# Performance work log

Measured on AMD Instinct MI355X. Metric: run time of the kernel, lower is better.

The kernel has to match this reference:

```python
import jax, jax.numpy as jnp
import numpy as np

L, B, D = 4096, 4, 1024

def setup_inputs() -> dict:
    key = jax.random.key(0)
    k1, k2, k3, k4 = jax.random.split(key, 4)
    return {
        "x": jax.random.normal(k1, (L, B, D), dtype=jnp.float32),
        "lmlg": jax.random.normal(k2, (D,), dtype=jnp.float32),
        "theta": jax.random.normal(k3, (D,), dtype=jnp.float32),
        "last_conv_init": jax.random.normal(k4, (D,), dtype=jnp.float32),
    }

def reference(x, lmlg, theta, last_conv_init):
    seq_len, batch, dim = x.shape
    # per-channel decay*rotation: c = gamma * e^{i*theta}, gamma = exp(-exp(lmlg))
    gamma = jnp.exp(-jnp.exp(lmlg))                       # [D]
    c = gamma * jnp.exp(1j * theta)                       # [D] complex64
    # causal filter c^n for n = 0..L-1
    n = jnp.arange(seq_len)[:, None]                      # [L,1]
    filt = c[None, :] ** n                                # [L,D] complex64
    # linear (causal) convolution via zero-padded FFT of length 2L
    filt_fft = jnp.fft.fft(filt, n=2 * seq_len, axis=0)   # [2L,D]
    x_fft = jnp.fft.fft(x, n=2 * seq_len, axis=0)         # [2L,B,D]
    conv_filter_x = jnp.fft.ifft(filt_fft[:, None, :] * x_fft, axis=0)[:seq_len]  # [L,B,D]
    # carry-in state (fresh state = last_conv_init expanded; detached in torch)
    last_conv = jax.lax.stop_gradient(
        jnp.broadcast_to(last_conv_init.astype(conv_filter_x.dtype), (batch, dim))
    )                                                     # [B,D]
    conv_with_past = conv_filter_x + last_conv[None, :, :] * filt[:, None, :] * c[None, None, :]
    return conv_with_past.real * x
```

## Files before the change

kernel.cpp:

```cpp
#include <hip/hip_runtime.h>


#define L_  4096
#define B_  4
#define D_  1024
#define BD_ (B_ * D_)
#define NC_ 128
#define CH_ (L_ / NC_)

template <int CH>
__global__ __launch_bounds__(256) void sc_sum(
    const float* __restrict__ x,
    const float* __restrict__ lmlg,
    const float* __restrict__ theta,
    float2* __restrict__ ws) {
  const int t   = threadIdx.x;
  const int bid = blockIdx.x;
  const int db  = bid & 3;
  const int b   = (bid >> 2) & (B_ - 1);
  const int k   = bid >> 4;
  const int d   = (db << 8) + t;

  const float lg = lmlg[d], th = theta[d];
  const float g  = expf(-expf(lg));
  const float cr = g * cosf(th), ci = g * sinf(th);

  float sr = 0.f, si = 0.f;
  const float* xp = x + (size_t)k * CH * BD_ + (size_t)b * D_ + d;
#pragma unroll 8
  for (int j = 0; j < CH; ++j) {
    float xv = xp[(size_t)j * BD_];
    float nr = fmaf(cr, sr, fmaf(-ci, si, xv));
    float ni = fmaf(cr, si, ci * sr);
    sr = nr; si = ni;
  }
  ws[(size_t)(k * B_ + b) * D_ + d] = make_float2(sr, si);
}

template <int CH>
__global__ __launch_bounds__(256) void sc_out(
    const float* __restrict__ x,
    const float* __restrict__ lmlg,
    const float* __restrict__ theta,
    const float* __restrict__ init,
    const float2* __restrict__ ws,
    float* __restrict__ out) {
  const int t   = threadIdx.x;
  const int bid = blockIdx.x;
  const int db  = bid & 3;
  const int b   = (bid >> 2) & (B_ - 1);
  const int k   = bid >> 4;
  const int d   = (db << 8) + t;

  const float lg = lmlg[d], th = theta[d];
  const float e  = expf(lg);
  const float g  = expf(-e);
  const float cr = g * cosf(th), ci = g * sinf(th);

  const float chf = (float)CH;
  const float G   = expf(-e * chf);
  const float Cr  = G * cosf(th * chf), Ci = G * sinf(th * chf);

  float hr = init[d], hi = 0.f;
  const float2* sp = ws + (size_t)b * D_ + d;
  {
    const float C2r = fmaf(Cr, Cr, -Ci * Ci);
    const float C2i = 2.f * Cr * Ci;
    int kk = 0;
    for (; kk + 2 <= k; kk += 2) {
      float2 s0 = sp[(size_t)kk * BD_];
      float2 s1 = sp[(size_t)(kk + 1) * BD_];
      float ur = fmaf(Cr, s0.x, fmaf(-Ci, s0.y, s1.x));
      float ui = fmaf(Cr, s0.y, fmaf( Ci, s0.x, s1.y));
      float nr = fmaf(C2r, hr, fmaf(-C2i, hi, ur));
      float ni = fmaf(C2r, hi, fmaf( C2i, hr, ui));
      hr = nr; hi = ni;
    }
    if (kk < k) {
      float2 s = sp[(size_t)kk * BD_];
      float nr = fmaf(Cr, hr, fmaf(-Ci, hi, s.x));
      float ni = fmaf(Cr, hi, fmaf( Ci, hr, s.y));
      hr = nr; hi = ni;
    }
  }

  const size_t off = (size_t)k * CH * BD_ + (size_t)b * D_ + d;
  const float* xp = x + off;
  float*       op = out + off;
#pragma unroll 8
  for (int j = 0; j < CH; ++j) {
    float xv = xp[(size_t)j * BD_];
    float nr = fmaf(cr, hr, fmaf(-ci, hi, xv));
    float ni = fmaf(cr, hi, ci * hr);
    hr = nr; hi = ni;
    __builtin_nontemporal_store(nr * xv, op + (size_t)j * BD_);
  }
}

__global__ __launch_bounds__(256) void sc_full(
    const float* __restrict__ x, const float* __restrict__ lmlg,
    const float* __restrict__ theta, const float* __restrict__ init,
    float* __restrict__ out) {
  const int idx = blockIdx.x * 256 + threadIdx.x;
  const int d   = idx & (D_ - 1);
  float g = expf(-expf(lmlg[d]));
  float cr = g * cosf(theta[d]), ci = g * sinf(theta[d]);
  float hr = init[d], hi = 0.f;
  const float* xp = x + idx;
  float*       op = out + idx;
  for (int n = 0; n < L_; ++n) {
    float xv = xp[(size_t)n * BD_];
    float nr = fmaf(cr, hr, fmaf(-ci, hi, xv));
    float ni = fmaf(cr, hi, ci * hr);
    hr = nr; hi = ni;
    op[(size_t)n * BD_] = nr * xv;
  }
}

extern "C" void kernel_launch(void* const* d_in, const int* in_sizes, int n_in,
                              void* d_out, int out_size, void* d_ws, size_t ws_size,
                              hipStream_t stream) {
  const float* x     = (const float*)d_in[0];
  const float* lmlg  = (const float*)d_in[1];
  const float* theta = (const float*)d_in[2];
  const float* init  = (const float*)d_in[3];
  float*  out = (float*)d_out;
  float2* ws  = (float2*)d_ws;

  const size_t need = (size_t)NC_ * B_ * D_ * sizeof(float2);
  if (ws_size >= need) {
    const int grid = NC_ * B_ * (D_ / 256);
    sc_sum<CH_><<<grid, 256, 0, stream>>>(x, lmlg, theta, ws);
    sc_out<CH_><<<grid, 256, 0, stream>>>(x, lmlg, theta, init, ws, out);
  } else {
    sc_full<<<BD_ / 256, 256, 0, stream>>>(x, lmlg, theta, init, out);
  }
}
```

Baseline: 134.3 us.

## Software-pipeline x loads with inline asm and stage outputs in LDS

Both scan kernels now issue global loads through inline assembly into two 8-register buffers, using explicit vmcnt waits and sched barriers to double-buffer them. This keeps 16 loads in flight while the serial complex recurrence runs. sc_out also writes its per-thread results into a 32x256 shared tile and then stores them as float4 rows instead of scalar nontemporal stores. The change assumes CH_ is 32, adds 32KB of LDS per block, which may reduce occupancy, and drops the nontemporal store hint.

```diff
diff --git a/kernel.cpp b/kernel.cpp
--- a/kernel.cpp
+++ b/kernel.cpp
@@ -1,4 +1,5 @@
 #include <hip/hip_runtime.h>
+#include <stdint.h>
 
 
 #define L_  4096
@@ -8,7 +9,12 @@
 #define NC_ 128
 #define CH_ (L_ / NC_)
 
-template <int CH>
+#define GLD(dst, addr) \
+  asm volatile("global_load_dword %0, %1, off" : "=v"(dst) : "v"(addr) : "memory")
+#define WAITV8() asm volatile("s_waitcnt vmcnt(8)" ::: "memory")
+#define WAITV0() asm volatile("s_waitcnt vmcnt(0)" ::: "memory")
+#define SCHEDB() __builtin_amdgcn_sched_barrier(0)
+
 __global__ __launch_bounds__(256) void sc_sum(
     const float* __restrict__ x,
     const float* __restrict__ lmlg,
@@ -25,19 +31,50 @@
   const float g  = expf(-expf(lg));
   const float cr = g * cosf(th), ci = g * sinf(th);
 
+  const float* xp = x + (size_t)k * CH_ * BD_ + (size_t)b * D_ + d;
+  float xa[8], xb[8];
+#pragma unroll
+  for (int u = 0; u < 8; ++u) GLD(xa[u], xp + (size_t)u * BD_);
+#pragma unroll
+  for (int u = 0; u < 8; ++u) GLD(xb[u], xp + (size_t)(8 + u) * BD_);
+
   float sr = 0.f, si = 0.f;
-  const float* xp = x + (size_t)k * CH * BD_ + (size_t)b * D_ + d;
-#pragma unroll 8
-  for (int j = 0; j < CH; ++j) {
-    float xv = xp[(size_t)j * BD_];
-    float nr = fmaf(cr, sr, fmaf(-ci, si, xv));
-    float ni = fmaf(cr, si, ci * sr);
-    sr = nr; si = ni;
-  }
+  WAITV8(); SCHEDB();
+#pragma unroll
+  for (int u = 0; u < 8; ++u) {
+    float nr = fmaf(cr, sr, fmaf(-ci, si, xa[u]));
+    float ni = fmaf(cr, si, ci * sr);
+    sr = nr; si = ni;
+  }
+#pragma unroll
+  for (int u = 0; u < 8; ++u) GLD(xa[u], xp + (size_t)(16 + u) * BD_);
+  WAITV8(); SCHEDB();
+#pragma unroll
+  for (int u = 0; u < 8; ++u) {
+    float nr = fmaf(cr, sr, fmaf(-ci, si, xb[u]));
+    float ni = fmaf(cr, si, ci * sr);
+    sr = nr; si = ni;
+  }
+#pragma unroll
+  for (int u = 0; u < 8; ++u) GLD(xb[u], xp + (size_t)(24 + u) * BD_);
+  WAITV8(); SCHEDB();
+#pragma unroll
+  for (int u = 0; u < 8; ++u) {
+    float nr = fmaf(cr, sr, fmaf(-ci, si, xa[u]));
+    float ni = fmaf(cr, si, ci * sr);
+    sr = nr; si = ni;
+  }
+  WAITV0(); SCHEDB();
+#pragma unroll
+  for (int u = 0; u < 8; ++u) {
+    float nr = fmaf(cr, sr, fmaf(-ci, si, xb[u]));
+    float ni = fmaf(cr, si, ci * sr);
+    sr = nr; si = ni;
+  }
+
   ws[(size_t)(k * B_ + b) * D_ + d] = make_float2(sr, si);
 }
 
-template <int CH>
 __global__ __launch_bounds__(256) void sc_out(
     const float* __restrict__ x,
     const float* __restrict__ lmlg,
@@ -45,6 +82,8 @@
     const float* __restrict__ init,
     const float2* __restrict__ ws,
     float* __restrict__ out) {
+  __shared__ float Ro[CH_][256];
+
   const int t   = threadIdx.x;
   const int bid = blockIdx.x;
   const int db  = bid & 3;
@@ -57,7 +96,7 @@
   const float g  = expf(-e);
   const float cr = g * cosf(th), ci = g * sinf(th);
 
-  const float chf = (float)CH;
+  const float chf = (float)CH_;
   const float G   = expf(-e * chf);
   const float Cr  = G * cosf(th * chf), Ci = G * sinf(th * chf);
 
@@ -84,16 +123,60 @@
     }
   }
 
-  const size_t off = (size_t)k * CH * BD_ + (size_t)b * D_ + d;
-  const float* xp = x + off;
-  float*       op = out + off;
-#pragma unroll 8
-  for (int j = 0; j < CH; ++j) {
-    float xv = xp[(size_t)j * BD_];
-    float nr = fmaf(cr, hr, fmaf(-ci, hi, xv));
-    float ni = fmaf(cr, hi, ci * hr);
-    hr = nr; hi = ni;
-    __builtin_nontemporal_store(nr * xv, op + (size_t)j * BD_);
+  const float* xp = x + (size_t)k * CH_ * BD_ + (size_t)b * D_ + d;
+  float xa[8], xb[8];
+#pragma unroll
+  for (int u = 0; u < 8; ++u) GLD(xa[u], xp + (size_t)u * BD_);
+#pragma unroll
+  for (int u = 0; u < 8; ++u) GLD(xb[u], xp + (size_t)(8 + u) * BD_);
+
+  WAITV8(); SCHEDB();
+#pragma unroll
+  for (int u = 0; u < 8; ++u) {
+    float nr = fmaf(cr, hr, fmaf(-ci, hi, xa[u]));
+    float ni = fmaf(cr, hi, ci * hr);
+    hr = nr; hi = ni;
+    Ro[u][t] = nr * xa[u];
+  }
+#pragma unroll
+  for (int u = 0; u < 8; ++u) GLD(xa[u], xp + (size_t)(16 + u) * BD_);
+  WAITV8(); SCHEDB();
+#pragma unroll
+  for (int u = 0; u < 8; ++u) {
+    float nr = fmaf(cr, hr, fmaf(-ci, hi, xb[u]));
+    float ni = fmaf(cr, hi, ci * hr);
+    hr = nr; hi = ni;
+    Ro[8 + u][t] = nr * xb[u];
+  }
+#pragma unroll
+  for (int u = 0; u < 8; ++u) GLD(xb[u], xp + (size_t)(24 + u) * BD_);
+  WAITV8(); SCHEDB();
+#pragma unroll
+  for (int u = 0; u < 8; ++u) {
+    float nr = fmaf(cr, hr, fmaf(-ci, hi, xa[u]));
+    float ni = fmaf(cr, hi, ci * hr);
+    hr = nr; hi = ni;
+    Ro[16 + u][t] = nr * xa[u];
+  }
+  WAITV0(); SCHEDB();
+#pragma unroll
+  for (int u = 0; u < 8; ++u) {
+    float nr = fmaf(cr, hr, fmaf(-ci, hi, xb[u]));
+    float ni = fmaf(cr, hi, ci * hr);
+    hr = nr; hi = ni;
+    Ro[24 + u][t] = nr * xb[u];
+  }
+
+  __syncthreads();
+
+  float* ob = out + (size_t)k * CH_ * BD_ + (size_t)b * D_ + (db << 8);
+  const int w    = t >> 6;
+  const int lane = t & 63;
+#pragma unroll
+  for (int u = 0; u < 8; ++u) {
+    const int r = w + u * 4;
+    float4 v = *(const float4*)&Ro[r][lane * 4];
+    *((float4*)(ob + (size_t)r * BD_) + lane) = v;
   }
 }
 
@@ -130,8 +213,8 @@
   const size_t need = (size_t)NC_ * B_ * D_ * sizeof(float2);
   if (ws_size >= need) {
     const int grid = NC_ * B_ * (D_ / 256);
-    sc_sum<CH_><<<grid, 256, 0, stream>>>(x, lmlg, theta, ws);
-    sc_out<CH_><<<grid, 256, 0, stream>>>(x, lmlg, theta, init, ws, out);
+    sc_sum<<<grid, 256, 0, stream>>>(x, lmlg, theta, ws);
+    sc_out<<<grid, 256, 0, stream>>>(x, lmlg, theta, init, ws, out);
   } else {
     sc_full<<<BD_ / 256, 256, 0, stream>>>(x, lmlg, theta, init, out);
   }
```

Result: no change. 136.6 us (+1.7%).
